# Kernel tuning notes

Measured on AMD Instinct MI355X. Metric: run time of the kernel, lower is better.

The kernel has to match this reference:

```python
import jax, jax.numpy as jnp
import numpy as np

N_TOKENS = 16384
D_MODEL = 1024
N_SEG = 4
H_SEG = 1024  # intermediate_size (4096) // num_segments


def setup_inputs() -> dict:
    key = jax.random.key(0)
    kx, ki, kg, ku, kd = jax.random.split(key, 5)
    x = jax.random.normal(kx, (N_TOKENS, D_MODEL), dtype=jnp.float32)
    token_segment_indices = jax.random.randint(ki, (N_TOKENS,), 0, N_SEG, dtype=jnp.int64)
    s = 1.0 / np.sqrt(D_MODEL)
    # weights stored [seg, in, out] for x @ W
    gate_w = jax.random.normal(kg, (N_SEG, D_MODEL, H_SEG), dtype=jnp.float32) * s
    up_w = jax.random.normal(ku, (N_SEG, D_MODEL, H_SEG), dtype=jnp.float32) * s
    down_w = jax.random.normal(kd, (N_SEG, H_SEG, D_MODEL), dtype=jnp.float32) * (1.0 / np.sqrt(H_SEG))
    return {
        'x': x,
        'gate_w': gate_w,
        'up_w': up_w,
        'down_w': down_w,
        'token_segment_indices': token_segment_indices,
    }


def reference(x, gate_w, up_w, down_w, token_segment_indices):
    # _forward_with_indices: each token is processed only by its assigned
    # segment's SwiGLU FFN; all other contributions are zero.  We compute each
    # segment densely and mask (jit-friendly, same math as gather->ffn->scatter).
    out = jnp.zeros_like(x)
    for s in range(N_SEG):
        hidden = jax.nn.silu(x @ gate_w[s]) * (x @ up_w[s])  # [N, H_SEG]
        y = hidden @ down_w[s]                                # [N, D_MODEL]
        mask = (token_segment_indices == s)[:, None]
        out = out + jnp.where(mask, y, 0.0)
    return out
```

## Files before the change

### kernel.cpp

```cpp
#include <hip/hip_runtime.h>
#include <hip/hip_bf16.h>
#include <math.h>

#define NT   16384
#define DM   1024
#define NSEG 4
#define BK   64
#define HS   1024
#define TBLN 68

typedef __attribute__((ext_vector_type(8))) short bf16x8;
typedef __attribute__((ext_vector_type(4))) float f32x4;

typedef __attribute__((address_space(1))) unsigned int gu32;
typedef __attribute__((address_space(3))) unsigned int lu32;

__device__ __forceinline__ void gll16(const void* g, void* l) {
  __builtin_amdgcn_global_load_lds((gu32*)(unsigned long long)g,
                                   (lu32*)(unsigned int)(unsigned long long)l,
                                   16, 0, 0);
}

__device__ __forceinline__ unsigned short cvt_bf16(float f) {
  unsigned int u = __float_as_uint(f);
  u += 0x7fffu + ((u >> 16) & 1u);
  return (unsigned short)(u >> 16);
}

__global__ __launch_bounds__(256) void k_prepw(
    const int* __restrict__ idx, int* __restrict__ part,
    const float* __restrict__ gw, const float* __restrict__ uw, const float* __restrict__ dw,
    unsigned short* __restrict__ gwt, unsigned short* __restrict__ uwt,
    unsigned short* __restrict__ dwt) {
  __shared__ float tile[64][65];
  const int bid = blockIdx.x, tid = threadIdx.x;
  if (bid < 64) {
    __shared__ int sc[5];
    if (tid < 5) sc[tid] = 0;
    __syncthreads();
    int lane = tid & 63;
    int w32 = idx[bid * 256 + tid];
    unsigned long long m = __ballot((tid & 1) && (w32 != 0));
    if (lane == 0 && m) atomicAdd(&sc[4], 1);
    __syncthreads();
    int is32 = (sc[4] != 0);
    int s = w32;
    if (!is32) s = idx[bid * 512 + 2 * tid];
#pragma unroll
    for (int q = 0; q < 4; ++q) {
      m = __ballot(s == q);
      if (lane == 0 && m) atomicAdd(&sc[q], (int)__popcll(m));
    }
    __syncthreads();
    if (tid < 4) part[bid * 8 + tid] = sc[tid];
    if (tid == 4) part[bid * 8 + 4] = is32;
    return;
  }
  int tb = bid - 64;
  int mtx = tb >> 10, seg = (tb >> 8) & 3, tl = tb & 255;
  const float* src = (mtx == 0 ? gw : mtx == 1 ? uw : dw) + (size_t)seg * DM * HS;
  unsigned short* dst = (mtx == 0 ? gwt : mtx == 1 ? uwt : dwt) + (size_t)seg * DM * HS;
  int n0 = (tl & 15) * 64, k0 = (tl >> 4) * 64;
  int col = tid & 63, rb = tid >> 6;
#pragma unroll
  for (int i = 0; i < 64; i += 4)
    tile[i + rb][col] = src[(size_t)(k0 + i + rb) * 1024 + n0 + col];
  __syncthreads();
  int kp = tid & 31, nb = tid >> 5;
#pragma unroll
  for (int j = 0; j < 64; j += 8) {
    int nn = j + nb;
    unsigned int w = (unsigned)cvt_bf16(tile[2 * kp][nn]) |
                     ((unsigned)cvt_bf16(tile[2 * kp + 1][nn]) << 16);
    *(unsigned int*)(dst + (size_t)(n0 + nn) * 1024 + k0 + 2 * kp) = w;
  }
}

__global__ __launch_bounds__(256) void k_cvtrank(
    const int* __restrict__ idx, const int* __restrict__ part,
    const float4* __restrict__ x,
    int* __restrict__ meta, int2* __restrict__ table,
    int* __restrict__ perm, uint4* __restrict__ xc) {
  __shared__ int cnt[64][4];
  __shared__ int wsum[4][4];
  __shared__ int tot[4], pref[4], gbase[4];
  __shared__ int rnk8[8];
  __shared__ int flag_s;
  const int tid = threadIdx.x, bid = blockIdx.x;
  const int lane = tid & 63, wv = tid >> 6;
  const int c = bid >> 5;
  const int p0 = (bid & 31) * 8;

  if (tid == 0) flag_s = part[c * 8 + 4];
  if (wv == 0) {
#pragma unroll
    for (int s = 0; s < 4; ++s) cnt[lane][s] = part[lane * 8 + s];
  }
  __syncthreads();
  const int is32 = flag_s;
  int tok = c * 256 + tid;
  int s_t = is32 ? idx[tok] : idx[2 * tok];
  int myr = 0;
  unsigned long long lt = (1ull << lane) - 1;
#pragma unroll
  for (int q = 0; q < 4; ++q) {
    unsigned long long m = __ballot(s_t == q);
    if (lane == 0) wsum[wv][q] = (int)__popcll(m);
    if (s_t == q) myr = (int)__popcll(m & lt);
  }
  __syncthreads();
  if (tid < 4) {
    int s = tid, t = 0, p = 0;
    for (int b = 0; b < 64; ++b) { if (b == c) p = t; t += cnt[b][s]; }
    tot[s] = t; pref[s] = p;
  }
  __syncthreads();
  if (tid == 0) {
    gbase[0] = 0;
    for (int s = 1; s < 4; ++s) gbase[s] = gbase[s - 1] + tot[s - 1];
    if (bid == 0) {
      int nt = 0;
      for (int s = 0; s < 4; ++s) {
        meta[s] = tot[s]; meta[5 + s] = gbase[s];
        for (int m0 = 0; m0 < tot[s]; m0 += 256) table[nt++] = make_int2(s, m0);
      }
      for (; nt < TBLN; ++nt) table[nt] = make_int2(-1, 0);
    }
  }
  __syncthreads();
  int wpre = 0;
  for (int w2 = 0; w2 < wv; ++w2) wpre += wsum[w2][s_t];
  int r = gbase[s_t] + pref[s_t] + wpre + myr;
  if (tid >= p0 && tid < p0 + 8) {
    perm[r] = tok;
    rnk8[tid - p0] = r;
  }
  __syncthreads();
  const int j = tid >> 5, l2 = tid & 31;
  const int tok8 = bid * 8 + j;
  const float4* src = x + (size_t)tok8 * 256;
  uint4* dst = xc + (size_t)rnk8[j] * 128;
#pragma unroll
  for (int it = 0; it < 4; ++it) {
    float4 a = src[it * 64 + l2 * 2];
    float4 b = src[it * 64 + l2 * 2 + 1];
    uint4 o;
    o.x = cvt_bf16(a.x) | ((unsigned)cvt_bf16(a.y) << 16);
    o.y = cvt_bf16(a.z) | ((unsigned)cvt_bf16(a.w) << 16);
    o.z = cvt_bf16(b.x) | ((unsigned)cvt_bf16(b.y) << 16);
    o.w = cvt_bf16(b.z) | ((unsigned)cvt_bf16(b.w) << 16);
    dst[it * 32 + l2] = o;
  }
}

#define WAITBAR_(N) \
  asm volatile("s_waitcnt vmcnt(" #N ") lgkmcnt(0)\n\ts_barrier" ::: "memory")
#define WAITBAR(N) WAITBAR_(N)

#define LDF(BUF, CUR, RB, F)                                               \
  F[0][0] = *(const bf16x8*)(&BUF[CUR][((RB) + fm) * 64] + x0);            \
  F[0][1] = *(const bf16x8*)(&BUF[CUR][((RB) + fm) * 64] + x1);            \
  F[1][0] = *(const bf16x8*)(&BUF[CUR][((RB) + 16 + fm) * 64] + x0);       \
  F[1][1] = *(const bf16x8*)(&BUF[CUR][((RB) + 16 + fm) * 64] + x1);

#define MM8(ACC, MH, NH, AF, BF)                                                                                            \
  __builtin_amdgcn_s_setprio(1);                                                                                            \
  ACC[2*(MH)+0][2*(NH)+0] = __builtin_amdgcn_mfma_f32_16x16x32_bf16(AF[0][0], BF[0][0], ACC[2*(MH)+0][2*(NH)+0], 0, 0, 0);  \
  ACC[2*(MH)+0][2*(NH)+1] = __builtin_amdgcn_mfma_f32_16x16x32_bf16(AF[0][0], BF[1][0], ACC[2*(MH)+0][2*(NH)+1], 0, 0, 0);  \
  ACC[2*(MH)+1][2*(NH)+0] = __builtin_amdgcn_mfma_f32_16x16x32_bf16(AF[1][0], BF[0][0], ACC[2*(MH)+1][2*(NH)+0], 0, 0, 0);  \
  ACC[2*(MH)+1][2*(NH)+1] = __builtin_amdgcn_mfma_f32_16x16x32_bf16(AF[1][0], BF[1][0], ACC[2*(MH)+1][2*(NH)+1], 0, 0, 0);  \
  ACC[2*(MH)+0][2*(NH)+0] = __builtin_amdgcn_mfma_f32_16x16x32_bf16(AF[0][1], BF[0][1], ACC[2*(MH)+0][2*(NH)+0], 0, 0, 0);  \
  ACC[2*(MH)+0][2*(NH)+1] = __builtin_amdgcn_mfma_f32_16x16x32_bf16(AF[0][1], BF[1][1], ACC[2*(MH)+0][2*(NH)+1], 0, 0, 0);  \
  ACC[2*(MH)+1][2*(NH)+0] = __builtin_amdgcn_mfma_f32_16x16x32_bf16(AF[1][1], BF[0][1], ACC[2*(MH)+1][2*(NH)+0], 0, 0, 0);  \
  ACC[2*(MH)+1][2*(NH)+1] = __builtin_amdgcn_mfma_f32_16x16x32_bf16(AF[1][1], BF[1][1], ACC[2*(MH)+1][2*(NH)+1], 0, 0, 0);  \
  __builtin_amdgcn_s_setprio(0);

__global__ __launch_bounds__(512) void k_gateup(
    const unsigned short* __restrict__ xc,
    const unsigned short* __restrict__ gwt,
    const unsigned short* __restrict__ uwt,
    const int* __restrict__ meta,
    const int2* __restrict__ table,
    unsigned short* __restrict__ hidden) {
  __shared__ __align__(16) unsigned short As[2][256 * BK];
  __shared__ __align__(16) unsigned short Bg[1][64 * BK];
  __shared__ __align__(16) unsigned short Bu[1][64 * BK];
  const int bid = blockIdx.x, tid = threadIdx.x;
  const int lb = (bid & 7) * (16 * TBLN / 8) + (bid >> 3);
  const int2 te = table[lb >> 4];
  if (te.x < 0) return;
  const int seg = te.x, m0 = te.y;
  const int count = meta[seg], base = meta[5 + seg];
  const int n0 = (lb & 15) * 64;

  const int lane = tid & 63;
  const int wv = tid >> 6;
  const int l0 = lane >> 3, j = lane & 7;

  const int rl0 = wv * 8, rl1 = 64 + wv * 8;
  const int rb0 = (rl0 & 31) + (rl0 >> 5) * 64;
  const int rb1 = (rl1 & 31) + (rl1 >> 5) * 64;
  const int a0d0 = rb0 * 128, a0d1 = rb1 * 128;
  const int a1d0 = a0d0 + 32 * 128, a1d1 = a0d1 + 32 * 128;
  const int r00 = rb0 + l0, r01 = rb1 + l0;
  const int r10 = r00 + 32, r11 = r01 + 32;
  auto rowof = [&](int r) { int g = m0 + r; return g < count ? g : count - 1; };
  const unsigned short* a0p0 = xc + (size_t)(base + rowof(r00)) * DM + (j ^ (r00 & 7)) * 8;
  const unsigned short* a0p1 = xc + (size_t)(base + rowof(r01)) * DM + (j ^ (r01 & 7)) * 8;
  const unsigned short* a1p0 = xc + (size_t)(base + rowof(r10)) * DM + (j ^ (r10 & 7)) * 8;
  const unsigned short* a1p1 = xc + (size_t)(base + rowof(r11)) * DM + (j ^ (r11 & 7)) * 8;
  const int nb = wv * 8 + l0;
  const unsigned short* gp  = gwt + (size_t)(seg * HS + n0 + nb) * DM + (j ^ (nb & 7)) * 8;
  const unsigned short* upp = uwt + (size_t)(seg * HS + n0 + nb) * DM + (j ^ (nb & 7)) * 8;
  const int bd = wv * 1024;

  const int wm = (wv & 3) * 64;
  const int wn = (wv >> 2) * 32;
  const int fm = lane & 15, fq = lane >> 4;
  const int x0 = (fq ^ (fm & 7)) * 8;
  const int x1 = ((4 + fq) ^ (fm & 7)) * 8;

  f32x4 accg[4][2] = {};
  f32x4 accu[4][2] = {};

#define GU_ITER(CUR, NXT) {                                   \
    bf16x8 af[2][2], af2[2][2], bg2[2][2], bu2[2][2];         \
    gll16(a0p0, (char*)&As[NXT][0] + a0d0);                   \
    gll16(a0p1, (char*)&As[NXT][0] + a0d1);                   \
    WAITBAR(5);                                               \
    LDF(As, CUR, wm, af); LDF(Bg, 0, wn, bg2);                \
    MM8(accg, 0, 0, af, bg2);                                 \
    WAITBAR(2);                                               \
    LDF(Bu, 0, wn, bu2);                                      \
    gll16(gp, (char*)&Bg[0][0] + bd);                         \
    MM8(accu, 0, 0, af, bu2);                                 \
    WAITBAR(3);                                               \
    LDF(As, CUR, wm + 32, af2);                               \
    gll16(a1p0, (char*)&As[NXT][0] + a1d0);                   \
    gll16(a1p1, (char*)&As[NXT][0] + a1d1);                   \
    gll16(upp, (char*)&Bu[0][0] + bd);                        \
    MM8(accg, 1, 0, af2, bg2);                                \
    MM8(accu, 1, 0, af2, bu2);                                \
    a0p0 += BK; a0p1 += BK; a1p0 += BK; a1p1 += BK; gp += BK; upp += BK; \
  }

  gll16(a0p0, (char*)&As[0][0] + a0d0);
  gll16(a0p1, (char*)&As[0][0] + a0d1);
  gll16(gp,   (char*)&Bg[0][0] + bd);
  gll16(a1p0, (char*)&As[0][0] + a1d0);
  gll16(a1p1, (char*)&As[0][0] + a1d1);
  gll16(upp,  (char*)&Bu[0][0] + bd);
  a0p0 += BK; a0p1 += BK; a1p0 += BK; a1p1 += BK; gp += BK; upp += BK;

#pragma unroll 1
  for (int t7 = 0; t7 < 7; ++t7) {
    GU_ITER(0, 1);
    GU_ITER(1, 0);
  }
  GU_ITER(0, 1);
  {
    bf16x8 af[2][2], af2[2][2], bg2[2][2], bu2[2][2];
    WAITBAR(3);
    LDF(As, 1, wm, af); LDF(Bg, 0, wn, bg2);
    MM8(accg, 0, 0, af, bg2);
    WAITBAR(0);
    LDF(Bu, 0, wn, bu2);
    MM8(accu, 0, 0, af, bu2);
    WAITBAR(0);
    LDF(As, 1, wm + 32, af2);
    MM8(accg, 1, 0, af2, bg2);
    MM8(accu, 1, 0, af2, bu2);
  }
#undef GU_ITER

  const int rq = fq * 4;
#pragma unroll
  for (int mi = 0; mi < 4; ++mi) {
#pragma unroll
    for (int r = 0; r < 4; ++r) {
      int row = m0 + wm + mi * 16 + rq + r;
      if (row < count) {
        unsigned short* h = hidden + (size_t)(base + row) * HS + n0 + wn;
#pragma unroll
        for (int ni = 0; ni < 2; ++ni) {
          float gv = accg[mi][ni][r];
          float uv = accu[mi][ni][r];
          float sig = 1.0f / (1.0f + __expf(-gv));
          h[ni * 16 + fm] = cvt_bf16(gv * sig * uv);
        }
      }
    }
  }
}

__global__ __launch_bounds__(512) void k_down(
    const unsigned short* __restrict__ hidden,
    const unsigned short* __restrict__ dwt,
    const int* __restrict__ meta,
    const int2* __restrict__ table,
    const int* __restrict__ perm,
    float* __restrict__ out) {
  __shared__ __align__(16) unsigned short As[2][256 * BK];
  __shared__ __align__(16) unsigned short Bs[1][128 * BK];
  const int bid = blockIdx.x, tid = threadIdx.x;
  const int lb = (bid & 7) * (8 * TBLN / 8) + (bid >> 3);
  const int2 te = table[lb >> 3];
  if (te.x < 0) return;
  const int seg = te.x, m0 = te.y;
  const int count = meta[seg], base = meta[5 + seg];
  const int n0 = (lb & 7) * 128;

  const int lane = tid & 63;
  const int wv = tid >> 6;
  const int l0 = lane >> 3, j = lane & 7;

  const int rl0 = wv * 8, rl1 = 64 + wv * 8;
  const int rb0 = (rl0 & 31) + (rl0 >> 5) * 64;
  const int rb1 = (rl1 & 31) + (rl1 >> 5) * 64;
  const int a0d0 = rb0 * 128, a0d1 = rb1 * 128;
  const int a1d0 = a0d0 + 32 * 128, a1d1 = a0d1 + 32 * 128;
  const int r00 = rb0 + l0, r01 = rb1 + l0;
  const int r10 = r00 + 32, r11 = r01 + 32;
  auto rowof = [&](int r) { int g = m0 + r; return g < count ? g : count - 1; };
  const unsigned short* a0p0 = hidden + (size_t)(base + rowof(r00)) * HS + (j ^ (r00 & 7)) * 8;
  const unsigned short* a0p1 = hidden + (size_t)(base + rowof(r01)) * HS + (j ^ (r01 & 7)) * 8;
  const unsigned short* a1p0 = hidden + (size_t)(base + rowof(r10)) * HS + (j ^ (r10 & 7)) * 8;
  const unsigned short* a1p1 = hidden + (size_t)(base + rowof(r11)) * HS + (j ^ (r11 & 7)) * 8;
  const int nl = wv * 8 + l0;
  const int nb0 = (nl & 31) + (nl >> 5) * 64;
  const int nb1 = nb0 + 32;
  const unsigned short* bp0 = dwt + (size_t)(seg * DM + n0 + nb0) * HS + (j ^ (nb0 & 7)) * 8;
  const unsigned short* bp1 = dwt + (size_t)(seg * DM + n0 + nb1) * HS + (j ^ (nb1 & 7)) * 8;
  const int bw = wv * 8;
  const int bd0 = ((bw & 31) + (bw >> 5) * 64) * 128;
  const int bd1 = bd0 + 32 * 128;

  const int wm = (wv & 3) * 64;
  const int wn = (wv >> 2) * 64;
  const int fm = lane & 15, fq = lane >> 4;
  const int x0 = (fq ^ (fm & 7)) * 8;
  const int x1 = ((4 + fq) ^ (fm & 7)) * 8;

  f32x4 acc[4][4] = {};

#define DN_ITER(CUR, NXT) {                                   \
    bf16x8 af[2][2], af2[2][2], b0[2][2], b1[2][2];           \
    gll16(a0p0, (char*)&As[NXT][0] + a0d0);                   \
    gll16(a0p1, (char*)&As[NXT][0] + a0d1);                   \
    WAITBAR(3);                                               \
    LDF(As, CUR, wm, af); LDF(Bs, 0, wn, b0);                 \
    MM8(acc, 0, 0, af, b0);                                   \
    WAITBAR(2);                                               \
    LDF(Bs, 0, wn + 32, b1);                                  \
    MM8(acc, 0, 1, af, b1);                                   \
    WAITBAR(2);                                               \
    LDF(As, CUR, wm + 32, af2);                               \
    gll16(a1p0, (char*)&As[NXT][0] + a1d0);                   \
    gll16(a1p1, (char*)&As[NXT][0] + a1d1);                   \
    gll16(bp0, (char*)&Bs[0][0] + bd0);                       \
    gll16(bp1, (char*)&Bs[0][0] + bd1);                       \
    MM8(acc, 1, 0, af2, b0);                                  \
    MM8(acc, 1, 1, af2, b1);                                  \
    a0p0 += BK; a0p1 += BK; a1p0 += BK; a1p1 += BK; bp0 += BK; bp1 += BK; \
  }

  gll16(a0p0, (char*)&As[0][0] + a0d0);
  gll16(a0p1, (char*)&As[0][0] + a0d1);
  gll16(a1p0, (char*)&As[0][0] + a1d0);
  gll16(a1p1, (char*)&As[0][0] + a1d1);
  gll16(bp0,  (char*)&Bs[0][0] + bd0);
  gll16(bp1,  (char*)&Bs[0][0] + bd1);
  a0p0 += BK; a0p1 += BK; a1p0 += BK; a1p1 += BK; bp0 += BK; bp1 += BK;

#pragma unroll 1
  for (int t7 = 0; t7 < 7; ++t7) {
    DN_ITER(0, 1);
    DN_ITER(1, 0);
  }
  DN_ITER(0, 1);
  {
    bf16x8 af[2][2], af2[2][2], b0[2][2], b1[2][2];
    WAITBAR(1);
    LDF(As, 1, wm, af); LDF(Bs, 0, wn, b0);
    MM8(acc, 0, 0, af, b0);
    WAITBAR(0);
    LDF(Bs, 0, wn + 32, b1);
    MM8(acc, 0, 1, af, b1);
    WAITBAR(0);
    LDF(As, 1, wm + 32, af2);
    MM8(acc, 1, 0, af2, b0);
    MM8(acc, 1, 1, af2, b1);
  }
#undef DN_ITER

  const int rq = fq * 4;
#pragma unroll
  for (int mi = 0; mi < 4; ++mi) {
#pragma unroll
    for (int r = 0; r < 4; ++r) {
      int row = m0 + wm + mi * 16 + rq + r;
      if (row < count) {
        int t = perm[base + row];
        float* o = out + (size_t)t * DM + n0 + wn;
#pragma unroll
        for (int ni = 0; ni < 4; ++ni)
          o[ni * 16 + fm] = acc[mi][ni][r];
      }
    }
  }
}


extern "C" void kernel_launch(void* const* d_in, const int* in_sizes, int n_in,
                              void* d_out, int out_size, void* d_ws, size_t ws_size,
                              hipStream_t stream) {
  const float* x  = (const float*)d_in[0];
  const float* gw = (const float*)d_in[1];
  const float* uw = (const float*)d_in[2];
  const float* dw = (const float*)d_in[3];
  const int* tsi  = (const int*)d_in[4];
  float* out = (float*)d_out;

  char* ws = (char*)d_ws;
  int*  meta  = (int*)ws;
  int*  part  = (int*)(ws + 256);
  int2* table = (int2*)(ws + 4096);
  int*  perm  = (int*)(ws + 8192);
  unsigned short* xc  = (unsigned short*)(ws + (1 << 18));
  unsigned short* gwt = xc + (size_t)NT * DM;
  unsigned short* uwt = gwt + (size_t)NSEG * HS * DM;
  unsigned short* dwt = uwt + (size_t)NSEG * HS * DM;
  unsigned short* hid = dwt + (size_t)NSEG * DM * HS;

  k_prepw<<<64 + 3072, 256, 0, stream>>>(tsi, part, gw, uw, dw, gwt, uwt, dwt);
  k_cvtrank<<<2048, 256, 0, stream>>>(tsi, part, (const float4*)x, meta, table, perm, (uint4*)xc);
  k_gateup<<<16 * TBLN, 512, 0, stream>>>(xc, gwt, uwt, meta, table, hid);
  k_down<<<8 * TBLN, 512, 0, stream>>>(hid, dwt, meta, table, perm, out);
}
```

Baseline: 311.5 us.

## Retile gate/up GEMM to 256x128 with triple-buffered BK32 and merge prep kernels

The gate/up kernel now computes a 256-row by 128-column output tile (64 gate plus 64 up columns, interleaved) per block, with half as many blocks. It uses a three-stage LDS ring of K=32 slices for A and B, replacing the old 256x64 tile that had a double-buffered A and single-buffered gate/up B. Each wave now holds 8x4 accumulators, which gives more A reuse per loaded B fragment. Separately, the small index scan is split into its own kernel and the weight transpose-convert is merged with the token rank and x conversion into one launch, so those two pieces of work can overlap. The cost is higher register pressure and more barriers per K step.

```diff
diff --git a/kernel.cpp b/kernel.cpp
--- a/kernel.cpp
+++ b/kernel.cpp
@@ -8,6 +8,7 @@
 #define BK   64
 #define HS   1024
 #define TBLN 68
+#define GGU  (8 * TBLN)
 
 typedef __attribute__((ext_vector_type(8))) short bf16x8;
 typedef __attribute__((ext_vector_type(4))) float f32x4;
@@ -27,66 +28,67 @@
   return (unsigned short)(u >> 16);
 }
 
-__global__ __launch_bounds__(256) void k_prepw(
-    const int* __restrict__ idx, int* __restrict__ part,
+__global__ __launch_bounds__(256) void k_scan(
+    const int* __restrict__ idx, int* __restrict__ part) {
+  __shared__ int sc[5];
+  const int bid = blockIdx.x, tid = threadIdx.x;
+  if (tid < 5) sc[tid] = 0;
+  __syncthreads();
+  int lane = tid & 63;
+  int w32 = idx[bid * 256 + tid];
+  unsigned long long m = __ballot((tid & 1) && (w32 != 0));
+  if (lane == 0 && m) atomicAdd(&sc[4], 1);
+  __syncthreads();
+  int is32 = (sc[4] != 0);
+  int s = w32;
+  if (!is32) s = idx[bid * 512 + 2 * tid];
+#pragma unroll
+  for (int q = 0; q < 4; ++q) {
+    m = __ballot(s == q);
+    if (lane == 0 && m) atomicAdd(&sc[q], (int)__popcll(m));
+  }
+  __syncthreads();
+  if (tid < 4) part[bid * 8 + tid] = sc[tid];
+  if (tid == 4) part[bid * 8 + 4] = is32;
+}
+
+__global__ __launch_bounds__(256) void k_prep(
+    const int* __restrict__ idx, const int* __restrict__ part,
+    const float4* __restrict__ x,
+    int* __restrict__ meta, int2* __restrict__ table,
+    int* __restrict__ perm, uint4* __restrict__ xc,
     const float* __restrict__ gw, const float* __restrict__ uw, const float* __restrict__ dw,
     unsigned short* __restrict__ gwt, unsigned short* __restrict__ uwt,
     unsigned short* __restrict__ dwt) {
   __shared__ float tile[64][65];
-  const int bid = blockIdx.x, tid = threadIdx.x;
-  if (bid < 64) {
-    __shared__ int sc[5];
-    if (tid < 5) sc[tid] = 0;
-    __syncthreads();
-    int lane = tid & 63;
-    int w32 = idx[bid * 256 + tid];
-    unsigned long long m = __ballot((tid & 1) && (w32 != 0));
-    if (lane == 0 && m) atomicAdd(&sc[4], 1);
-    __syncthreads();
-    int is32 = (sc[4] != 0);
-    int s = w32;
-    if (!is32) s = idx[bid * 512 + 2 * tid];
-#pragma unroll
-    for (int q = 0; q < 4; ++q) {
-      m = __ballot(s == q);
-      if (lane == 0 && m) atomicAdd(&sc[q], (int)__popcll(m));
-    }
-    __syncthreads();
-    if (tid < 4) part[bid * 8 + tid] = sc[tid];
-    if (tid == 4) part[bid * 8 + 4] = is32;
-    return;
-  }
-  int tb = bid - 64;
-  int mtx = tb >> 10, seg = (tb >> 8) & 3, tl = tb & 255;
-  const float* src = (mtx == 0 ? gw : mtx == 1 ? uw : dw) + (size_t)seg * DM * HS;
-  unsigned short* dst = (mtx == 0 ? gwt : mtx == 1 ? uwt : dwt) + (size_t)seg * DM * HS;
-  int n0 = (tl & 15) * 64, k0 = (tl >> 4) * 64;
-  int col = tid & 63, rb = tid >> 6;
-#pragma unroll
-  for (int i = 0; i < 64; i += 4)
-    tile[i + rb][col] = src[(size_t)(k0 + i + rb) * 1024 + n0 + col];
-  __syncthreads();
-  int kp = tid & 31, nb = tid >> 5;
-#pragma unroll
-  for (int j = 0; j < 64; j += 8) {
-    int nn = j + nb;
-    unsigned int w = (unsigned)cvt_bf16(tile[2 * kp][nn]) |
-                     ((unsigned)cvt_bf16(tile[2 * kp + 1][nn]) << 16);
-    *(unsigned int*)(dst + (size_t)(n0 + nn) * 1024 + k0 + 2 * kp) = w;
-  }
-}
-
-__global__ __launch_bounds__(256) void k_cvtrank(
-    const int* __restrict__ idx, const int* __restrict__ part,
-    const float4* __restrict__ x,
-    int* __restrict__ meta, int2* __restrict__ table,
-    int* __restrict__ perm, uint4* __restrict__ xc) {
   __shared__ int cnt[64][4];
   __shared__ int wsum[4][4];
   __shared__ int tot[4], pref[4], gbase[4];
   __shared__ int rnk8[8];
   __shared__ int flag_s;
-  const int tid = threadIdx.x, bid = blockIdx.x;
+  const int tid = threadIdx.x;
+  if (blockIdx.x >= 2048) {
+    int tb = blockIdx.x - 2048;
+    int mtx = tb >> 10, seg = (tb >> 8) & 3, tl = tb & 255;
+    const float* src = (mtx == 0 ? gw : mtx == 1 ? uw : dw) + (size_t)seg * DM * HS;
+    unsigned short* dst = (mtx == 0 ? gwt : mtx == 1 ? uwt : dwt) + (size_t)seg * DM * HS;
+    int n0 = (tl & 15) * 64, k0 = (tl >> 4) * 64;
+    int col = tid & 63, rb = tid >> 6;
+#pragma unroll
+    for (int i = 0; i < 64; i += 4)
+      tile[i + rb][col] = src[(size_t)(k0 + i + rb) * 1024 + n0 + col];
+    __syncthreads();
+    int kp = tid & 31, nb = tid >> 5;
+#pragma unroll
+    for (int j = 0; j < 64; j += 8) {
+      int nn = j + nb;
+      unsigned int w = (unsigned)cvt_bf16(tile[2 * kp][nn]) |
+                       ((unsigned)cvt_bf16(tile[2 * kp + 1][nn]) << 16);
+      *(unsigned int*)(dst + (size_t)(n0 + nn) * 1024 + k0 + 2 * kp) = w;
+    }
+    return;
+  }
+  const int bid = blockIdx.x;
   const int lane = tid & 63, wv = tid >> 6;
   const int c = bid >> 5;
   const int p0 = (bid & 31) * 8;
@@ -156,6 +158,8 @@
 #define WAITBAR_(N) \
   asm volatile("s_waitcnt vmcnt(" #N ") lgkmcnt(0)\n\ts_barrier" ::: "memory")
 #define WAITBAR(N) WAITBAR_(N)
+#define SBAR() __builtin_amdgcn_s_barrier()
+#define LGKM0() asm volatile("s_waitcnt lgkmcnt(0)" ::: "memory")
 
 #define LDF(BUF, CUR, RB, F)                                               \
   F[0][0] = *(const bf16x8*)(&BUF[CUR][((RB) + fm) * 64] + x0);            \
@@ -182,111 +186,120 @@
     const int* __restrict__ meta,
     const int2* __restrict__ table,
     unsigned short* __restrict__ hidden) {
-  __shared__ __align__(16) unsigned short As[2][256 * BK];
-  __shared__ __align__(16) unsigned short Bg[1][64 * BK];
-  __shared__ __align__(16) unsigned short Bu[1][64 * BK];
+  __shared__ __align__(16) unsigned short As[3][256 * 32];
+  __shared__ __align__(16) unsigned short Bs[3][256 * 32];
   const int bid = blockIdx.x, tid = threadIdx.x;
-  const int lb = (bid & 7) * (16 * TBLN / 8) + (bid >> 3);
-  const int2 te = table[lb >> 4];
+  const int lb = (bid & 7) * (GGU / 8) + (bid >> 3);
+  const int2 te = table[lb >> 3];
   if (te.x < 0) return;
   const int seg = te.x, m0 = te.y;
   const int count = meta[seg], base = meta[5 + seg];
-  const int n0 = (lb & 15) * 64;
-
-  const int lane = tid & 63;
-  const int wv = tid >> 6;
-  const int l0 = lane >> 3, j = lane & 7;
-
-  const int rl0 = wv * 8, rl1 = 64 + wv * 8;
-  const int rb0 = (rl0 & 31) + (rl0 >> 5) * 64;
-  const int rb1 = (rl1 & 31) + (rl1 >> 5) * 64;
-  const int a0d0 = rb0 * 128, a0d1 = rb1 * 128;
-  const int a1d0 = a0d0 + 32 * 128, a1d1 = a0d1 + 32 * 128;
-  const int r00 = rb0 + l0, r01 = rb1 + l0;
-  const int r10 = r00 + 32, r11 = r01 + 32;
-  auto rowof = [&](int r) { int g = m0 + r; return g < count ? g : count - 1; };
-  const unsigned short* a0p0 = xc + (size_t)(base + rowof(r00)) * DM + (j ^ (r00 & 7)) * 8;
-  const unsigned short* a0p1 = xc + (size_t)(base + rowof(r01)) * DM + (j ^ (r01 & 7)) * 8;
-  const unsigned short* a1p0 = xc + (size_t)(base + rowof(r10)) * DM + (j ^ (r10 & 7)) * 8;
-  const unsigned short* a1p1 = xc + (size_t)(base + rowof(r11)) * DM + (j ^ (r11 & 7)) * 8;
-  const int nb = wv * 8 + l0;
-  const unsigned short* gp  = gwt + (size_t)(seg * HS + n0 + nb) * DM + (j ^ (nb & 7)) * 8;
-  const unsigned short* upp = uwt + (size_t)(seg * HS + n0 + nb) * DM + (j ^ (nb & 7)) * 8;
-  const int bd = wv * 1024;
-
-  const int wm = (wv & 3) * 64;
-  const int wn = (wv >> 2) * 32;
+  const int n0 = (lb & 7) * 128;
+
+  const int lane = tid & 63, wv = tid >> 6;
+  const int mi = wv >> 2, ng = wv & 3;
   const int fm = lane & 15, fq = lane >> 4;
-  const int x0 = (fq ^ (fm & 7)) * 8;
-  const int x1 = ((4 + fq) ^ (fm & 7)) * 8;
-
-  f32x4 accg[4][2] = {};
-  f32x4 accu[4][2] = {};
-
-#define GU_ITER(CUR, NXT) {                                   \
-    bf16x8 af[2][2], af2[2][2], bg2[2][2], bu2[2][2];         \
-    gll16(a0p0, (char*)&As[NXT][0] + a0d0);                   \
-    gll16(a0p1, (char*)&As[NXT][0] + a0d1);                   \
-    WAITBAR(5);                                               \
-    LDF(As, CUR, wm, af); LDF(Bg, 0, wn, bg2);                \
-    MM8(accg, 0, 0, af, bg2);                                 \
-    WAITBAR(2);                                               \
-    LDF(Bu, 0, wn, bu2);                                      \
-    gll16(gp, (char*)&Bg[0][0] + bd);                         \
-    MM8(accu, 0, 0, af, bu2);                                 \
-    WAITBAR(3);                                               \
-    LDF(As, CUR, wm + 32, af2);                               \
-    gll16(a1p0, (char*)&As[NXT][0] + a1d0);                   \
-    gll16(a1p1, (char*)&As[NXT][0] + a1d1);                   \
-    gll16(upp, (char*)&Bu[0][0] + bd);                        \
-    MM8(accg, 1, 0, af2, bg2);                                \
-    MM8(accu, 1, 0, af2, bu2);                                \
-    a0p0 += BK; a0p1 += BK; a1p0 += BK; a1p1 += BK; gp += BK; upp += BK; \
-  }
-
-  gll16(a0p0, (char*)&As[0][0] + a0d0);
-  gll16(a0p1, (char*)&As[0][0] + a0d1);
-  gll16(gp,   (char*)&Bg[0][0] + bd);
-  gll16(a1p0, (char*)&As[0][0] + a1d0);
-  gll16(a1p1, (char*)&As[0][0] + a1d1);
-  gll16(upp,  (char*)&Bu[0][0] + bd);
-  a0p0 += BK; a0p1 += BK; a1p0 += BK; a1p1 += BK; gp += BK; upp += BK;
+  const int laneRd = (fm >> 1) * 128 + (((((fm & 1) << 2) | fq)) ^ (fm >> 1)) * 16;
+
+  const unsigned short *aS0, *aS1, *bS0, *bS1;
+  int aO0, aO1, bO0, bO1;
+  {
+    int o0 = wv * 1024 + lane * 16;
+    int o1 = 8192 + o0;
+    int rp0 = o0 >> 7, jj0 = ((o0 >> 4) & 7) ^ (rp0 & 7);
+    int rp1 = o1 >> 7, jj1 = ((o1 >> 4) & 7) ^ (rp1 & 7);
+    int pr0 = rp0 * 2 + (jj0 >> 2), j20 = jj0 & 3;
+    int pr1 = rp1 * 2 + (jj1 >> 2), j21 = jj1 & 3;
+    int ga0 = m0 + pr0; ga0 = ga0 < count ? ga0 : count - 1;
+    int ga1 = m0 + pr1; ga1 = ga1 < count ? ga1 : count - 1;
+    aS0 = xc + (size_t)(base + ga0) * DM + j20 * 8;  aO0 = o0;
+    aS1 = xc + (size_t)(base + ga1) * DM + j21 * 8;  aO1 = o1;
+    int nc0 = n0 + (pr0 >> 5) * 16 + (pr0 & 15);
+    int nc1 = n0 + (pr1 >> 5) * 16 + (pr1 & 15);
+    bS0 = (((pr0 >> 4) & 1) ? uwt : gwt) + (size_t)(seg * HS + nc0) * DM + j20 * 8;  bO0 = o0;
+    bS1 = (((pr1 >> 4) & 1) ? uwt : gwt) + (size_t)(seg * HS + nc1) * DM + j21 * 8;  bO1 = o1;
+  }
+
+  f32x4 acc[8][4] = {};
+
+#define GU_SA(B) { gll16(aS0, (char*)&As[B][0] + aO0); gll16(aS1, (char*)&As[B][0] + aO1); aS0 += 32; aS1 += 32; }
+#define GU_SB(B) { gll16(bS0, (char*)&Bs[B][0] + bO0); gll16(bS1, (char*)&Bs[B][0] + bO1); bS0 += 32; bS1 += 32; }
+
+#define GU_PH1(C, STMT) {                                                   \
+    const char* Ab = (const char*)&As[C][0];                                \
+    const char* Bb = (const char*)&Bs[C][0];                                \
+    _Pragma("unroll")                                                       \
+    for (int f = 0; f < 4; ++f)                                             \
+      afr[f] = *(const bf16x8*)(Ab + (mi * 128 + f * 16) * 64 + laneRd);    \
+    _Pragma("unroll")                                                       \
+    for (int f = 0; f < 4; ++f)                                             \
+      bfr[f] = *(const bf16x8*)(Bb + (ng * 64 + f * 16) * 64 + laneRd);     \
+    STMT;                                                                   \
+    SBAR(); LGKM0();                                                        \
+    __builtin_amdgcn_s_setprio(1);                                          \
+    _Pragma("unroll")                                                       \
+    for (int f = 0; f < 4; ++f)                                             \
+      _Pragma("unroll")                                                     \
+      for (int n = 0; n < 4; ++n)                                           \
+        acc[f][n] = __builtin_amdgcn_mfma_f32_16x16x32_bf16(afr[f], bfr[n], acc[f][n], 0, 0, 0); \
+    __builtin_amdgcn_s_setprio(0);                                          \
+    SBAR(); }
+
+#define GU_PH2(C, STMT, GN) {                                               \
+    const char* Ab = (const char*)&As[C][0];                                \
+    _Pragma("unroll")                                                       \
+    for (int f = 0; f < 4; ++f)                                             \
+      afr[f] = *(const bf16x8*)(Ab + (mi * 128 + 64 + f * 16) * 64 + laneRd); \
+    STMT;                                                                   \
+    SBAR(); LGKM0();                                                        \
+    __builtin_amdgcn_s_setprio(1);                                          \
+    _Pragma("unroll")                                                       \
+    for (int f = 0; f < 4; ++f)                                             \
+      _Pragma("unroll")                                                     \
+      for (int n = 0; n < 4; ++n)                                           \
+        acc[4 + f][n] = __builtin_amdgcn_mfma_f32_16x16x32_bf16(afr[f], bfr[n], acc[4 + f][n], 0, 0, 0); \
+    __builtin_amdgcn_s_setprio(0);                                          \
+    WAITBAR(GN); }
+
+#define GU_TILE(C, P) { bf16x8 afr[4], bfr[4];                              \
+    GU_PH1(C, GU_SA(P)); GU_PH2(C, GU_SB(P), 4); }
+#define GU_TILE_E(C, GN) { bf16x8 afr[4], bfr[4];                           \
+    GU_PH1(C, ); GU_PH2(C, , GN); }
+
+  asm volatile("s_waitcnt vmcnt(0)" ::: "memory");
+  GU_SA(0); GU_SB(0);
+  GU_SA(1); GU_SB(1);
+  WAITBAR(4);
 
 #pragma unroll 1
-  for (int t7 = 0; t7 < 7; ++t7) {
-    GU_ITER(0, 1);
-    GU_ITER(1, 0);
-  }
-  GU_ITER(0, 1);
-  {
-    bf16x8 af[2][2], af2[2][2], bg2[2][2], bu2[2][2];
-    WAITBAR(3);
-    LDF(As, 1, wm, af); LDF(Bg, 0, wn, bg2);
-    MM8(accg, 0, 0, af, bg2);
-    WAITBAR(0);
-    LDF(Bu, 0, wn, bu2);
-    MM8(accu, 0, 0, af, bu2);
-    WAITBAR(0);
-    LDF(As, 1, wm + 32, af2);
-    MM8(accg, 1, 0, af2, bg2);
-    MM8(accu, 1, 0, af2, bu2);
-  }
-#undef GU_ITER
-
-  const int rq = fq * 4;
-#pragma unroll
-  for (int mi = 0; mi < 4; ++mi) {
+  for (int g3 = 0; g3 < 10; ++g3) {
+    GU_TILE(0, 2);
+    GU_TILE(1, 0);
+    GU_TILE(2, 1);
+  }
+  GU_TILE_E(0, 0);
+  GU_TILE_E(1, 0);
+#undef GU_TILE
+#undef GU_TILE_E
+#undef GU_PH1
+#undef GU_PH2
+#undef GU_SA
+#undef GU_SB
+
+#pragma unroll
+  for (int mf = 0; mf < 8; ++mf) {
 #pragma unroll
     for (int r = 0; r < 4; ++r) {
-      int row = m0 + wm + mi * 16 + rq + r;
+      int row = m0 + mi * 128 + mf * 16 + fq * 4 + r;
       if (row < count) {
-        unsigned short* h = hidden + (size_t)(base + row) * HS + n0 + wn;
-#pragma unroll
-        for (int ni = 0; ni < 2; ++ni) {
-          float gv = accg[mi][ni][r];
-          float uv = accu[mi][ni][r];
+        unsigned short* h = hidden + (size_t)(base + row) * HS;
+#pragma unroll
+        for (int q = 0; q < 2; ++q) {
+          int ncol = n0 + (ng * 2 + q) * 16 + fm;
+          float gv = acc[mf][2 * q][r];
+          float uv = acc[mf][2 * q + 1][r];
           float sig = 1.0f / (1.0f + __expf(-gv));
-          h[ni * 16 + fm] = cvt_bf16(gv * sig * uv);
+          h[ncol] = cvt_bf16(gv * sig * uv);
         }
       }
     }
@@ -432,8 +445,9 @@
   unsigned short* dwt = uwt + (size_t)NSEG * HS * DM;
   unsigned short* hid = dwt + (size_t)NSEG * DM * HS;
 
-  k_prepw<<<64 + 3072, 256, 0, stream>>>(tsi, part, gw, uw, dw, gwt, uwt, dwt);
-  k_cvtrank<<<2048, 256, 0, stream>>>(tsi, part, (const float4*)x, meta, table, perm, (uint4*)xc);
-  k_gateup<<<16 * TBLN, 512, 0, stream>>>(xc, gwt, uwt, meta, table, hid);
+  k_scan<<<64, 256, 0, stream>>>(tsi, part);
+  k_prep<<<2048 + 3072, 256, 0, stream>>>(tsi, part, (const float4*)x, meta, table,
+                                          perm, (uint4*)xc, gw, uw, dw, gwt, uwt, dwt);
+  k_gateup<<<GGU, 512, 0, stream>>>(xc, gwt, uwt, meta, table, hid);
   k_down<<<8 * TBLN, 512, 0, stream>>>(hid, dwt, meta, table, perm, out);
 }
```

Result: slower. 320.0 us (+2.7%).
